# Optimization experiments

Measured on AMD Instinct MI355X. Metric: run time of the kernel, lower is better.

## Reference

```python
import jax, jax.numpy as jnp
import numpy as np

B, DV, W, H = 128, 2048, 14, 14
S = W * H            # 196 spatial positions
DQ = 2048            # question vector dim
DA = 1200            # attention dim_v == dim_q == dim_mm (MLB elementwise fusion)
G = 4                # nb_glimpses
DH = 2048            # fusion dim_h (total); per-glimpse = DH // G
NANS = 3000


def setup_inputs() -> dict:
    key = jax.random.key(0)
    ks = jax.random.split(key, 16)
    s = 0.02
    return {
        "input_v": jax.random.normal(ks[0], (B, DV, W, H), jnp.float32),
        "x_q_vec": jax.random.normal(ks[1], (B, DQ), jnp.float32),
        # conv_v_att: 1x1 conv DV->DA  (expressed as channel matmul)
        "Wv_att": jax.random.normal(ks[2], (DV, DA), jnp.float32) * s,
        "bv_att": jnp.zeros((DA,), jnp.float32),
        # linear_q_att: DQ->DA
        "Wq_att": jax.random.normal(ks[3], (DQ, DA), jnp.float32) * s,
        "bq_att": jnp.zeros((DA,), jnp.float32),
        # conv_att: 1x1 conv DA->G
        "Wa": jax.random.normal(ks[4], (DA, G), jnp.float32) * s,
        "ba": jnp.zeros((G,), jnp.float32),
        # per-glimpse fusion linears DV -> DH//G, stacked over glimpses
        "Wf": jax.random.normal(ks[5], (G, DV, DH // G), jnp.float32) * s,
        "bf": jnp.zeros((G, DH // G), jnp.float32),
        # linear_q_fusion: DQ -> DH
        "Wqf": jax.random.normal(ks[6], (DQ, DH), jnp.float32) * s,
        "bqf": jnp.zeros((DH,), jnp.float32),
        # linear_classif: DH -> NANS
        "Wc": jax.random.normal(ks[7], (DH, NANS), jnp.float32) * s,
        "bc": jnp.zeros((NANS,), jnp.float32),
    }


def reference(input_v, x_q_vec, Wv_att, bv_att, Wq_att, bq_att, Wa, ba,
              Wf, bf, Wqf, bqf, Wc, bc):
    b = input_v.shape[0]
    v_flat = input_v.reshape(b, DV, S)                      # [B, DV, S]

    # --- attention scores ---
    # conv_v_att (1x1) + tanh -> [B, S, DA]
    x_v = jnp.tanh(jnp.einsum('bcs,cd->bsd', v_flat, Wv_att) + bv_att)
    # linear_q_att + tanh -> [B, DA], broadcast over spatial
    x_q = jnp.tanh(x_q_vec @ Wq_att + bq_att)
    # MLB fusion_att: elementwise multiply, then tanh (activation_mm)
    x_att = jnp.tanh(x_v * x_q[:, None, :])                 # [B, S, DA]
    scores = jnp.einsum('bsd,dg->bsg', x_att, Wa) + ba      # [B, S, G]
    att = jax.nn.softmax(scores, axis=1)                    # softmax over spatial

    # --- weighted pooling per glimpse ---
    v_att = jnp.einsum('bsg,bcs->bgc', att, v_flat)         # [B, G, DV]

    # --- fusion of glimpses ---
    xv = jnp.tanh(jnp.einsum('bgc,gch->bgh', v_att, Wf) + bf)  # [B, G, DH/G]
    xv = xv.reshape(b, DH)                                   # concat glimpses
    xq = jnp.tanh(x_q_vec @ Wqf + bqf)                       # [B, DH]
    x = xv * xq                                              # MLB fusion_classif

    # --- classifier ---
    x = jnp.tanh(x)
    return x @ Wc + bc                                       # [B, NANS]
```

## Files before the change

kernel.cpp:

```cpp
#include <hip/hip_runtime.h>
#include <hip/hip_bf16.h>

#define BB   128
#define DV   2048
#define SS   196
#define DQ   2048
#define DA   1200
#define DAP  1280
#define GG   4
#define DH   2048
#define NANS 3000
#define NANSP 3008
#define MROWS (BB*SS)
#define NT   5
#define KSPLIT 8
#define KCHUNK (DV/KSPLIT)
#define NQ   (DAP + DH)

typedef __attribute__((ext_vector_type(8))) short bf16x8;
typedef __attribute__((ext_vector_type(4))) float f32x4;

__device__ __forceinline__ float fast_tanh(float x) {
    float e = __expf(2.0f * x);
    return 1.0f - 2.0f * __builtin_amdgcn_rcpf(e + 1.0f);
}

__device__ __forceinline__ void async_copy16(const void* gsrc, void* ldst) {
    __builtin_amdgcn_global_load_lds(
        (const __attribute__((address_space(1))) void*)gsrc,
        (__attribute__((address_space(3))) void*)ldst, 16, 0, 0);
}

__global__ void pad_misc(const float* __restrict__ bv, const float* __restrict__ Wa,
                         float* __restrict__ bvp, float* __restrict__ wap) {
    int i = blockIdx.x * 256 + threadIdx.x;
    if (i < DAP) bvp[i] = (i < DA) ? bv[i] : 0.f;
    if (i < DAP * GG) {
        int d = i >> 2;
        wap[i] = (d < DA) ? Wa[i] : 0.f;
    }
}

__global__ __launch_bounds__(256) void transpose_v(const float* __restrict__ v,
                                                   __hip_bfloat16* __restrict__ vt) {
    const int b    = blockIdx.z;
    const int t    = threadIdx.x;
    const int lane = t & 63;
    const int w    = t >> 6;
    const int sl   = lane >> 2;
    const int cq   = lane & 3;
    const int s    = blockIdx.y * 16 + sl;
    const int c0   = blockIdx.x * 128 + w * 32 + cq * 8;
    if (s >= SS) return;
    const float* src = v + (size_t)b * DV * SS + (size_t)c0 * SS + s;
    float f[8];
#pragma unroll
    for (int i = 0; i < 8; ++i) f[i] = src[(size_t)i * SS];
    union { bf16x8 v8; __hip_bfloat16 h[8]; } u;
#pragma unroll
    for (int i = 0; i < 8; ++i) u.h[i] = __float2bfloat16(f[i]);
    *(bf16x8*)(vt + ((size_t)b * SS + s) * DV + c0) = u.v8;
}

__global__ __launch_bounds__(256) void transpose_w(const float* __restrict__ Wv,
                                                   __hip_bfloat16* __restrict__ wvt) {
    __shared__ float tile[64][65];
    const int d0 = blockIdx.x * 64;
    const int c0 = blockIdx.y * 64;
    const int t  = threadIdx.x;
    const int col  = t & 63;
    const int rowb = t >> 6;
#pragma unroll
    for (int i = 0; i < 16; ++i) {
        int c = rowb + i * 4;
        int d = d0 + col;
        tile[c][col] = (d < DA) ? Wv[(size_t)(c0 + c) * DA + d] : 0.f;
    }
    __syncthreads();
#pragma unroll
    for (int i = 0; i < 16; ++i) {
        int dl = rowb + i * 4;
        wvt[(size_t)(d0 + dl) * DV + c0 + col] = __float2bfloat16(tile[col][dl]);
    }
}

template <int SEL>
__global__ __launch_bounds__(256) void gemm_partial(
    const float* __restrict__ A, int lda,
    const float* __restrict__ Bm, const float* __restrict__ B2,
    float* __restrict__ Cp, int Npad) {
    __shared__ float As[64 * 132];
    __shared__ float Bs[64 * 68];
    const int t     = threadIdx.x;
    const int n0    = blockIdx.x * 64;
    const int kbase = blockIdx.y * KCHUNK;

    const float* Aeff = A;
    const float* Beff;
    int ldb, ncol0, nlim;
    if (SEL == 0) {
        Beff = Bm; ldb = NANS; ncol0 = n0; nlim = NANS;
    } else if (SEL == 1) {
        int gg = n0 >> 9;
        Aeff = A + gg * 2048;
        Beff = Bm + (size_t)gg * 2048 * 512;
        ldb = 512; ncol0 = n0 & 511; nlim = 1 << 30;
    } else {
        if (n0 < DAP) { Beff = Bm; ldb = DA; ncol0 = n0;      nlim = DA; }
        else          { Beff = B2; ldb = DH; ncol0 = n0 - DAP; nlim = 1 << 30; }
    }

    const int tm = (t & 31) * 4;
    const int tn = (t >> 5) * 8;
    float acc[4][8] = {};

    for (int k0 = kbase; k0 < kbase + KCHUNK; k0 += 64) {
        {
            int kk = t & 63, mb = (t >> 6) * 32;
#pragma unroll
            for (int i = 0; i < 32; ++i)
                As[kk * 132 + mb + i] = Aeff[(size_t)(mb + i) * lda + k0 + kk];
        }
        {
            int j = t & 63, kr = t >> 6;
            bool ok = (ncol0 + j) < nlim;
#pragma unroll
            for (int i = 0; i < 16; ++i) {
                int k = kr + i * 4;
                Bs[k * 68 + j] = ok ? Beff[(size_t)(k0 + k) * ldb + ncol0 + j] : 0.f;
            }
        }
        __syncthreads();
#pragma unroll
        for (int kk = 0; kk < 64; ++kk) {
            const float4 av = *(const float4*)(As + kk * 132 + tm);
            const float4 b0 = *(const float4*)(Bs + kk * 68 + tn);
            const float4 b1 = *(const float4*)(Bs + kk * 68 + tn + 4);
            const float am[4] = {av.x, av.y, av.z, av.w};
#pragma unroll
            for (int i = 0; i < 4; ++i) {
                acc[i][0] += am[i] * b0.x; acc[i][1] += am[i] * b0.y;
                acc[i][2] += am[i] * b0.z; acc[i][3] += am[i] * b0.w;
                acc[i][4] += am[i] * b1.x; acc[i][5] += am[i] * b1.y;
                acc[i][6] += am[i] * b1.z; acc[i][7] += am[i] * b1.w;
            }
        }
        __syncthreads();
    }
#pragma unroll
    for (int i = 0; i < 4; ++i) {
        size_t base = ((size_t)blockIdx.y * 128 + tm + i) * Npad + n0 + tn;
        float4 v0 = {acc[i][0], acc[i][1], acc[i][2], acc[i][3]};
        float4 v1 = {acc[i][4], acc[i][5], acc[i][6], acc[i][7]};
        *(float4*)(Cp + base) = v0;
        *(float4*)(Cp + base + 4) = v1;
    }
}

template <int MODE>
__global__ __launch_bounds__(256) void gemm_epilogue(
    const float* __restrict__ Cp, int Npad, int Nreal,
    const float* __restrict__ bias, const float* __restrict__ aux,
    float* __restrict__ out, int ldo) {
    int n = blockIdx.x * 256 + threadIdx.x;
    int m = blockIdx.y;
    if (n >= Npad) return;
    float s = 0.f;
#pragma unroll
    for (int ks = 0; ks < KSPLIT; ++ks)
        s += Cp[((size_t)ks * 128 + m) * Npad + n];
    if (MODE == 0) {
        if (n >= Nreal) return;
        out[(size_t)m * ldo + n] = s + bias[n];
    } else {
        float xv = fast_tanh(s + bias[n]);
        out[(size_t)m * ldo + n] = fast_tanh(xv * aux[(size_t)m * 2048 + n]);
    }
}

__global__ __launch_bounds__(256) void epilogue_q(
    const float* __restrict__ Cp,
    const float* __restrict__ bqa, const float* __restrict__ bqf,
    float* __restrict__ qatt, float* __restrict__ qfus) {
    int n = blockIdx.x * 256 + threadIdx.x;
    int m = blockIdx.y;
    if (n >= NQ) return;
    float s = 0.f;
#pragma unroll
    for (int ks = 0; ks < KSPLIT; ++ks)
        s += Cp[((size_t)ks * 128 + m) * NQ + n];
    if (n < DAP) {
        qatt[(size_t)m * DAP + n] = (n < DA) ? fast_tanh(s + bqa[n]) : 0.f;
    } else {
        int j = n - DAP;
        qfus[(size_t)m * DH + j] = fast_tanh(s + bqf[j]);
    }
}

__global__ __launch_bounds__(512, 2) void big_gemm(
    const __hip_bfloat16* __restrict__ vt,
    const __hip_bfloat16* __restrict__ wt,
    const float* __restrict__ bvp,
    const float* __restrict__ qatt,
    const float* __restrict__ wap,
    float* __restrict__ scores_p) {
    __shared__ __align__(16) char lds[131072];
    __shared__ __align__(16) float wa_s[256 * 4];
    __shared__ float qs[3 * 256];

    const int t    = threadIdx.x;
    const int lane = t & 63;
    const int w    = t >> 6;
    const int wr   = w >> 2;
    const int wc   = w & 3;

    int bid = blockIdx.x;
    int grp = bid / 40, r = bid % 40;
    int mt, nt;
    if (grp < 12) { mt = grp * 8 + (r & 7); nt = r >> 3; }
    else          { mt = 96 + (r & 1);      nt = r >> 1; }
    const int m0 = mt * 256, n0 = nt * 256;
    const int b_lo = m0 / SS;
    const int bs1  = (b_lo + 1) * SS;
    const int bs2  = (b_lo + 2) * SS;

    if (t < 256) *(float4*)(wa_s + t * 4) = *(const float4*)(wap + (n0 + t) * 4);
    {
        int j = t >> 8, c = t & 255;
        int b = b_lo + j;
        qs[t] = (b < BB) ? qatt[(size_t)b * DAP + n0 + c] : 0.f;
        if (t < 256) {
            int b2 = b_lo + 2;
            qs[512 + t] = (b2 < BB) ? qatt[(size_t)b2 * DAP + n0 + t] : 0.f;
        }
    }
    __syncthreads();

    const int srow   = t >> 2;
    const int schunk = (t & 3) ^ ((t >> 3) & 3);
    const __hip_bfloat16* aG = vt + (size_t)(m0 + srow) * DV + schunk * 8;
    const __hip_bfloat16* bG = wt + (size_t)(n0 + srow) * DV + schunk * 8;

    auto STAGE_ITEM = [&](int k, int p) {
        const int ks = p >> 1, mat = p & 1;
        const __hip_bfloat16* g = (mat ? bG : aG) + (size_t)k * 64 + ks * 32;
        char* dst = lds + (k & 1) * 65536 + ks * 32768 + mat * 16384 + t * 16;
        async_copy16(g, dst);
        async_copy16(g + (size_t)128 * DV, dst + 8192);
    };

    const int rchk = ((lane >> 4) ^ (((lane & 15) >> 1) & 3)) * 16;
    const int aRow = (wr * 128 + (lane & 15)) * 64;
    const int bRow = (wc * 64 + (lane & 15)) * 64;

    f32x4 acc[8][4];
#pragma unroll
    for (int i = 0; i < 8; ++i)
#pragma unroll
        for (int j = 0; j < 4; ++j) acc[i][j] = (f32x4){0.f, 0.f, 0.f, 0.f};

    STAGE_ITEM(0, 0); STAGE_ITEM(0, 1);
    STAGE_ITEM(0, 2); STAGE_ITEM(0, 3);
    STAGE_ITEM(1, 0);
    asm volatile("s_waitcnt vmcnt(6)" ::: "memory");
    __builtin_amdgcn_s_barrier();

    for (int kt = 0; kt < 32; ++kt) {
        const int cur = kt & 1;
        const char* Xb = lds + cur * 65536;
        bf16x8 bfr[4];
#pragma unroll
        for (int p = 0; p < 4; ++p) {
            const int ks = p >> 1, mh = p & 1;
            const char* Ar = Xb + ks * 32768;
            bf16x8 afr[4];
#pragma unroll
            for (int q = 0; q < 4; ++q)
                afr[q] = *(const bf16x8*)(Ar + aRow + (mh * 64 + q * 16) * 64 + rchk);
            if (mh == 0) {
#pragma unroll
                for (int ni = 0; ni < 4; ++ni)
                    bfr[ni] = *(const bf16x8*)(Ar + 16384 + bRow + (ni * 16) * 64 + rchk);
            }
            if (p < 3) {
                if (kt < 31) STAGE_ITEM(kt + 1, p + 1);
            } else {
                if (kt < 30) STAGE_ITEM(kt + 2, 0);
            }
            if (p == 1) {
                if (kt < 31) asm volatile("s_waitcnt vmcnt(6)" ::: "memory");
                else         asm volatile("s_waitcnt vmcnt(0)" ::: "memory");
            } else if (p == 3) {
                if (kt < 30)       asm volatile("s_waitcnt vmcnt(6)" ::: "memory");
                else if (kt == 30) asm volatile("s_waitcnt vmcnt(4)" ::: "memory");
                else               asm volatile("s_waitcnt vmcnt(0)" ::: "memory");
            }
            __builtin_amdgcn_s_barrier();
            __builtin_amdgcn_s_setprio(1);
#pragma unroll
            for (int q = 0; q < 4; ++q)
#pragma unroll
                for (int ni = 0; ni < 4; ++ni)
                    acc[mh * 4 + q][ni] = __builtin_amdgcn_mfma_f32_16x16x32_bf16(
                        afr[q], bfr[ni], acc[mh * 4 + q][ni], 0, 0, 0);
            __builtin_amdgcn_s_setprio(0);
        }
    }

    __syncthreads();
    float* sc = (float*)lds;

    const int colb_l = wc * 64 + (lane & 15);
    const int colb_g = n0 + colb_l;
    float bvv[4];
    float4 wv[4];
#pragma unroll
    for (int ni = 0; ni < 4; ++ni) {
        bvv[ni] = bvp[colb_g + ni * 16];
        wv[ni]  = *(const float4*)(wa_s + (colb_l + ni * 16) * 4);
    }
#pragma unroll
    for (int mi = 0; mi < 8; ++mi) {
#pragma unroll
        for (int rr = 0; rr < 4; ++rr) {
            int lrow = wr * 128 + mi * 16 + ((lane >> 4) << 2) + rr;
            int row  = m0 + lrow;
            int qoff = (row >= bs1 ? 256 : 0) + (row >= bs2 ? 256 : 0);
            float p0 = 0.f, p1 = 0.f, p2 = 0.f, p3 = 0.f;
#pragma unroll
            for (int ni = 0; ni < 4; ++ni) {
                float xv = fast_tanh(acc[mi][ni][rr] + bvv[ni]);
                float xa = fast_tanh(xv * qs[qoff + colb_l + ni * 16]);
                p0 += xa * wv[ni].x; p1 += xa * wv[ni].y;
                p2 += xa * wv[ni].z; p3 += xa * wv[ni].w;
            }
#pragma unroll
            for (int mk = 1; mk < 16; mk <<= 1) {
                p0 += __shfl_xor(p0, mk); p1 += __shfl_xor(p1, mk);
                p2 += __shfl_xor(p2, mk); p3 += __shfl_xor(p3, mk);
            }
            if ((lane & 15) == 0)
                *(float4*)(sc + ((size_t)wc * 256 + lrow) * 4) =
                    (float4){p0, p1, p2, p3};
        }
    }
    __syncthreads();
    if (t < 256) {
        float4 s0 = *(float4*)(sc + (0 * 256 + t) * 4);
        float4 s1 = *(float4*)(sc + (1 * 256 + t) * 4);
        float4 s2 = *(float4*)(sc + (2 * 256 + t) * 4);
        float4 s3 = *(float4*)(sc + (3 * 256 + t) * 4);
        float4 s = {s0.x + s1.x + s2.x + s3.x, s0.y + s1.y + s2.y + s3.y,
                    s0.z + s1.z + s2.z + s3.z, s0.w + s1.w + s2.w + s3.w};
        *(float4*)(scores_p + ((size_t)nt * MROWS + m0 + t) * 4) = s;
    }
}

__global__ __launch_bounds__(256) void softmax_pool(
    const float* __restrict__ scores_p,
    const __hip_bfloat16* __restrict__ vt,
    float* __restrict__ vatt) {
    __shared__ __align__(16) float att[SS * GG];
    const int b = blockIdx.y;
    const int t = threadIdx.x;
    if (t < SS) {
        float4 s = {0.f, 0.f, 0.f, 0.f};
#pragma unroll
        for (int ntile = 0; ntile < NT; ++ntile) {
            float4 p = *(const float4*)(scores_p + ((size_t)ntile * MROWS + b * SS + t) * 4);
            s.x += p.x; s.y += p.y; s.z += p.z; s.w += p.w;
        }
        *(float4*)(att + t * 4) = s;
    }
    __syncthreads();
    {
        const int g = t >> 6;
        const int lane = t & 63;
        float mx = -3.0e38f;
        for (int s = lane; s < SS; s += 64) mx = fmaxf(mx, att[s * 4 + g]);
#pragma unroll
        for (int m = 32; m > 0; m >>= 1) mx = fmaxf(mx, __shfl_xor(mx, m));
        float sum = 0.f;
        for (int s = lane; s < SS; s += 64) sum += __expf(att[s * 4 + g] - mx);
#pragma unroll
        for (int m = 32; m > 0; m >>= 1) sum += __shfl_xor(sum, m);
        float inv = __builtin_amdgcn_rcpf(sum);
        for (int s = lane; s < SS; s += 64) att[s * 4 + g] = __expf(att[s * 4 + g] - mx) * inv;
    }
    __syncthreads();
    const int c = blockIdx.x * 1024 + t * 4;
    const __hip_bfloat16* vp = vt + (size_t)b * SS * DV + c;
    float a0[4] = {}, a1[4] = {}, a2[4] = {}, a3[4] = {};
#pragma unroll 4
    for (int s = 0; s < SS; ++s) {
        uint2 u = *(const uint2*)(vp + (size_t)s * DV);
        float v0 = __uint_as_float(u.x << 16);
        float v1 = __uint_as_float(u.x & 0xffff0000u);
        float v2 = __uint_as_float(u.y << 16);
        float v3 = __uint_as_float(u.y & 0xffff0000u);
        float4 aw = *(const float4*)(att + s * 4);
        a0[0] += v0 * aw.x; a0[1] += v0 * aw.y; a0[2] += v0 * aw.z; a0[3] += v0 * aw.w;
        a1[0] += v1 * aw.x; a1[1] += v1 * aw.y; a1[2] += v1 * aw.z; a1[3] += v1 * aw.w;
        a2[0] += v2 * aw.x; a2[1] += v2 * aw.y; a2[2] += v2 * aw.z; a2[3] += v2 * aw.w;
        a3[0] += v3 * aw.x; a3[1] += v3 * aw.y; a3[2] += v3 * aw.z; a3[3] += v3 * aw.w;
    }
    float* vb = vatt + (size_t)b * GG * DV;
#pragma unroll
    for (int g = 0; g < GG; ++g) {
        float4 o = {a0[g], a1[g], a2[g], a3[g]};
        *(float4*)(vb + (size_t)g * DV + c) = o;
    }
}

extern "C" void kernel_launch(void* const* d_in, const int* in_sizes, int n_in,
                              void* d_out, int out_size, void* d_ws, size_t ws_size,
                              hipStream_t stream) {
    const float* input_v = (const float*)d_in[0];
    const float* x_q     = (const float*)d_in[1];
    const float* Wv      = (const float*)d_in[2];
    const float* bv      = (const float*)d_in[3];
    const float* Wq_att  = (const float*)d_in[4];
    const float* bq_att  = (const float*)d_in[5];
    const float* Wa      = (const float*)d_in[6];
    const float* Wf      = (const float*)d_in[8];
    const float* bf_     = (const float*)d_in[9];
    const float* Wqf     = (const float*)d_in[10];
    const float* bqf     = (const float*)d_in[11];
    const float* Wc      = (const float*)d_in[12];
    const float* bc      = (const float*)d_in[13];
    float* out = (float*)d_out;

    char* wsb = (char*)d_ws;
    size_t off = 0;
    auto carve = [&](size_t bytes) -> void* {
        void* p = wsb + off;
        off += (bytes + 255) & ~(size_t)255;
        return p;
    };
    __hip_bfloat16* vt  = (__hip_bfloat16*)carve((size_t)MROWS * DV * 2);
    __hip_bfloat16* wvt = (__hip_bfloat16*)carve((size_t)DAP * DV * 2);
    float* Cp       = (float*)carve((size_t)KSPLIT * 128 * NQ * 4);
    float* scores_p = (float*)carve((size_t)NT * MROWS * GG * 4);
    float* qatt = (float*)carve((size_t)BB * DAP * 4);
    float* qfus = (float*)carve((size_t)BB * DH * 4);
    float* bvp  = (float*)carve((size_t)DAP * 4);
    float* wap  = (float*)carve((size_t)DAP * GG * 4);
    float* vatt = (float*)carve((size_t)BB * GG * DV * 4);
    float* xbuf = (float*)carve((size_t)BB * DH * 4);
    (void)ws_size; (void)n_in; (void)in_sizes; (void)out_size;

    pad_misc<<<dim3(20), 256, 0, stream>>>(bv, Wa, bvp, wap);
    transpose_v<<<dim3(DV / 128, 13, BB), 256, 0, stream>>>(input_v, vt);
    transpose_w<<<dim3(DAP / 64, DV / 64), 256, 0, stream>>>(Wv, wvt);

    gemm_partial<2><<<dim3(NQ / 64, KSPLIT), 256, 0, stream>>>(
        x_q, DQ, Wq_att, Wqf, Cp, NQ);
    epilogue_q<<<dim3(NQ / 256, BB), 256, 0, stream>>>(Cp, bq_att, bqf, qatt, qfus);

    big_gemm<<<dim3(490), 512, 0, stream>>>(vt, wvt, bvp, qatt, wap, scores_p);

    softmax_pool<<<dim3(2, BB), 256, 0, stream>>>(scores_p, vt, vatt);

    gemm_partial<1><<<dim3(DH / 64, KSPLIT), 256, 0, stream>>>(
        vatt, GG * DV, Wf, nullptr, Cp, DH);
    gemm_epilogue<2><<<dim3(DH / 256, BB), 256, 0, stream>>>(
        Cp, DH, DH, bf_, qfus, xbuf, DH);

    gemm_partial<0><<<dim3(NANSP / 64, KSPLIT), 256, 0, stream>>>(
        xbuf, DH, Wc, nullptr, Cp, NANSP);
    gemm_epilogue<0><<<dim3(NANSP / 256 + 1, BB), 256, 0, stream>>>(
        Cp, NANSP, NANS, bc, nullptr, out, NANS);
}
```

Baseline: 642.4 us.

## Merge front-end prep kernels into one launch, vectorize GEMM tile loads, trim barriers

Combines the padding, weight transpose and question GEMM kernels into a single launch that dispatches on block index, cutting launch count and letting those independent jobs fill the GPU together. The small fp32 GEMM now loads its A and B tiles with float4 global reads instead of scalar ones, at the cost of strided scalar LDS writes for the transposed A tile. In the big MFMA GEMM the per-phase barrier now runs only on the phases that wait for loads, which removes two barriers per k-tile. This relies on the LDS reuse pattern staying race-free without them.

```diff
diff --git a/kernel.cpp b/kernel.cpp
--- a/kernel.cpp
+++ b/kernel.cpp
@@ -31,16 +31,6 @@
         (__attribute__((address_space(3))) void*)ldst, 16, 0, 0);
 }
 
-__global__ void pad_misc(const float* __restrict__ bv, const float* __restrict__ Wa,
-                         float* __restrict__ bvp, float* __restrict__ wap) {
-    int i = blockIdx.x * 256 + threadIdx.x;
-    if (i < DAP) bvp[i] = (i < DA) ? bv[i] : 0.f;
-    if (i < DAP * GG) {
-        int d = i >> 2;
-        wap[i] = (d < DA) ? Wa[i] : 0.f;
-    }
-}
-
 __global__ __launch_bounds__(256) void transpose_v(const float* __restrict__ v,
                                                    __hip_bfloat16* __restrict__ vt) {
     const int b    = blockIdx.z;
@@ -62,38 +52,15 @@
     *(bf16x8*)(vt + ((size_t)b * SS + s) * DV + c0) = u.v8;
 }
 
-__global__ __launch_bounds__(256) void transpose_w(const float* __restrict__ Wv,
-                                                   __hip_bfloat16* __restrict__ wvt) {
-    __shared__ float tile[64][65];
-    const int d0 = blockIdx.x * 64;
-    const int c0 = blockIdx.y * 64;
-    const int t  = threadIdx.x;
-    const int col  = t & 63;
-    const int rowb = t >> 6;
-#pragma unroll
-    for (int i = 0; i < 16; ++i) {
-        int c = rowb + i * 4;
-        int d = d0 + col;
-        tile[c][col] = (d < DA) ? Wv[(size_t)(c0 + c) * DA + d] : 0.f;
-    }
-    __syncthreads();
-#pragma unroll
-    for (int i = 0; i < 16; ++i) {
-        int dl = rowb + i * 4;
-        wvt[(size_t)(d0 + dl) * DV + c0 + col] = __float2bfloat16(tile[col][dl]);
-    }
-}
-
 template <int SEL>
-__global__ __launch_bounds__(256) void gemm_partial(
+__device__ __forceinline__ void gemm_body(
+    int bx, int by, int t,
     const float* __restrict__ A, int lda,
     const float* __restrict__ Bm, const float* __restrict__ B2,
-    float* __restrict__ Cp, int Npad) {
-    __shared__ float As[64 * 132];
-    __shared__ float Bs[64 * 68];
-    const int t     = threadIdx.x;
-    const int n0    = blockIdx.x * 64;
-    const int kbase = blockIdx.y * KCHUNK;
+    float* __restrict__ Cp, int Npad,
+    float* As, float* Bs) {
+    const int n0    = bx * 64;
+    const int kbase = by * KCHUNK;
 
     const float* Aeff = A;
     const float* Beff;
@@ -112,22 +79,32 @@
 
     const int tm = (t & 31) * 4;
     const int tn = (t >> 5) * 8;
+    const int sm = t >> 1, kq = t & 1;
+    const int bk = t >> 4, bn4 = (t & 15) * 4;
+    const bool bok = (ncol0 + bn4 + 3) < nlim;
     float acc[4][8] = {};
 
     for (int k0 = kbase; k0 < kbase + KCHUNK; k0 += 64) {
         {
-            int kk = t & 63, mb = (t >> 6) * 32;
-#pragma unroll
-            for (int i = 0; i < 32; ++i)
-                As[kk * 132 + mb + i] = Aeff[(size_t)(mb + i) * lda + k0 + kk];
+            const float* Ap = Aeff + (size_t)sm * lda + k0 + kq * 32;
+#pragma unroll
+            for (int i = 0; i < 8; ++i) {
+                float4 a4 = *(const float4*)(Ap + i * 4);
+                int kk = kq * 32 + i * 4;
+                As[(kk + 0) * 132 + sm] = a4.x;
+                As[(kk + 1) * 132 + sm] = a4.y;
+                As[(kk + 2) * 132 + sm] = a4.z;
+                As[(kk + 3) * 132 + sm] = a4.w;
+            }
         }
         {
-            int j = t & 63, kr = t >> 6;
-            bool ok = (ncol0 + j) < nlim;
-#pragma unroll
-            for (int i = 0; i < 16; ++i) {
-                int k = kr + i * 4;
-                Bs[k * 68 + j] = ok ? Beff[(size_t)(k0 + k) * ldb + ncol0 + j] : 0.f;
+#pragma unroll
+            for (int i = 0; i < 4; ++i) {
+                int k = bk + i * 16;
+                float4 b4 = bok
+                    ? *(const float4*)(Beff + (size_t)(k0 + k) * ldb + ncol0 + bn4)
+                    : (float4){0.f, 0.f, 0.f, 0.f};
+                *(float4*)(Bs + k * 68 + bn4) = b4;
             }
         }
         __syncthreads();
@@ -149,12 +126,67 @@
     }
 #pragma unroll
     for (int i = 0; i < 4; ++i) {
-        size_t base = ((size_t)blockIdx.y * 128 + tm + i) * Npad + n0 + tn;
+        size_t base = ((size_t)by * 128 + tm + i) * Npad + n0 + tn;
         float4 v0 = {acc[i][0], acc[i][1], acc[i][2], acc[i][3]};
         float4 v1 = {acc[i][4], acc[i][5], acc[i][6], acc[i][7]};
         *(float4*)(Cp + base) = v0;
         *(float4*)(Cp + base + 4) = v1;
     }
+}
+
+template <int SEL>
+__global__ __launch_bounds__(256) void gemm_partial(
+    const float* __restrict__ A, int lda,
+    const float* __restrict__ Bm, const float* __restrict__ B2,
+    float* __restrict__ Cp, int Npad) {
+    __shared__ __align__(16) float As[64 * 132];
+    __shared__ __align__(16) float Bs[64 * 68];
+    gemm_body<SEL>(blockIdx.x, blockIdx.y, threadIdx.x, A, lda, Bm, B2, Cp,
+                   Npad, As, Bs);
+}
+
+__global__ __launch_bounds__(256) void front_pack(
+    const float* __restrict__ bv, const float* __restrict__ Wa,
+    float* __restrict__ bvp, float* __restrict__ wap,
+    const float* __restrict__ Wv, __hip_bfloat16* __restrict__ wvt,
+    const float* __restrict__ x_q, const float* __restrict__ Wq_att,
+    const float* __restrict__ Wqf, float* __restrict__ Cp) {
+    __shared__ __align__(16) float shmem[64 * 132 + 64 * 68];
+    const int t = threadIdx.x;
+    int bid = blockIdx.x;
+    if (bid < 20) {
+        int i = bid * 256 + t;
+        if (i < DAP) bvp[i] = (i < DA) ? bv[i] : 0.f;
+        if (i < DAP * GG) {
+            int d = i >> 2;
+            wap[i] = (d < DA) ? Wa[i] : 0.f;
+        }
+        return;
+    }
+    bid -= 20;
+    if (bid < 640) {
+        float (*tile)[65] = (float(*)[65])shmem;
+        const int d0 = (bid % 20) * 64;
+        const int c0 = (bid / 20) * 64;
+        const int col  = t & 63;
+        const int rowb = t >> 6;
+#pragma unroll
+        for (int i = 0; i < 16; ++i) {
+            int c = rowb + i * 4;
+            int d = d0 + col;
+            tile[c][col] = (d < DA) ? Wv[(size_t)(c0 + c) * DA + d] : 0.f;
+        }
+        __syncthreads();
+#pragma unroll
+        for (int i = 0; i < 16; ++i) {
+            int dl = rowb + i * 4;
+            wvt[(size_t)(d0 + dl) * DV + c0 + col] = __float2bfloat16(tile[col][dl]);
+        }
+        return;
+    }
+    bid -= 640;
+    gemm_body<2>(bid % 52, bid / 52, t, x_q, DQ, Wq_att, Wqf, Cp, NQ,
+                 shmem, shmem + 64 * 132);
 }
 
 template <int MODE>
@@ -290,12 +322,13 @@
             if (p == 1) {
                 if (kt < 31) asm volatile("s_waitcnt vmcnt(6)" ::: "memory");
                 else         asm volatile("s_waitcnt vmcnt(0)" ::: "memory");
+                __builtin_amdgcn_s_barrier();
             } else if (p == 3) {
                 if (kt < 30)       asm volatile("s_waitcnt vmcnt(6)" ::: "memory");
                 else if (kt == 30) asm volatile("s_waitcnt vmcnt(4)" ::: "memory");
                 else               asm volatile("s_waitcnt vmcnt(0)" ::: "memory");
-            }
-            __builtin_amdgcn_s_barrier();
+                __builtin_amdgcn_s_barrier();
+            }
             __builtin_amdgcn_s_setprio(1);
 #pragma unroll
             for (int q = 0; q < 4; ++q)
@@ -449,12 +482,10 @@
     float* xbuf = (float*)carve((size_t)BB * DH * 4);
     (void)ws_size; (void)n_in; (void)in_sizes; (void)out_size;
 
-    pad_misc<<<dim3(20), 256, 0, stream>>>(bv, Wa, bvp, wap);
     transpose_v<<<dim3(DV / 128, 13, BB), 256, 0, stream>>>(input_v, vt);
-    transpose_w<<<dim3(DAP / 64, DV / 64), 256, 0, stream>>>(Wv, wvt);
-
-    gemm_partial<2><<<dim3(NQ / 64, KSPLIT), 256, 0, stream>>>(
-        x_q, DQ, Wq_att, Wqf, Cp, NQ);
+
+    front_pack<<<dim3(1076), 256, 0, stream>>>(
+        bv, Wa, bvp, wap, Wv, wvt, x_q, Wq_att, Wqf, Cp);
     epilogue_q<<<dim3(NQ / 256, BB), 256, 0, stream>>>(Cp, bq_att, bqf, qatt, qfus);
 
     big_gemm<<<dim3(490), 512, 0, stream>>>(vt, wvt, bvp, qatt, wap, scores_p);
```

Result: faster. 625.4 us (-2.6%).
